# Kernel tuning notes

Hardware: AMD Instinct MI355X
Metric: run time of the kernel (lower is better)

## Reference

```python
import jax, jax.numpy as jnp
import numpy as np

N = 100000      # nodes
E = 3200000     # edges (avg degree 32)
G = 64          # graphs in batch
IN_C = 128      # in_channels
HID = 16        # hidden_channels
OUT_C = 8       # out_channels
EDGE_C = 16     # edge_channels


def setup_inputs() -> dict:
    key = jax.random.key(0)
    ks = jax.random.split(key, 10)
    x = jax.random.normal(ks[0], (N, IN_C), dtype=jnp.float32)
    edge_index = jax.random.randint(ks[1], (2, E), 0, N, dtype=jnp.int64)
    edge_attr = jax.random.normal(ks[2], (E, EDGE_C), dtype=jnp.float32)
    batch_index = jnp.sort(jax.random.randint(ks[3], (N,), 0, G, dtype=jnp.int64))
    def lin(k, fan_in, fan_out):
        bound = 1.0 / np.sqrt(fan_in)
        return jax.random.uniform(k, (fan_in, fan_out), jnp.float32, -bound, bound)
    return {
        "x": x,
        "edge_index": edge_index,
        "edge_attr": edge_attr,
        "batch_index": batch_index,
        "W1_node": lin(ks[4], IN_C, HID),
        "W1_edge": lin(ks[5], EDGE_C, HID),
        "W2_node": lin(ks[6], HID, HID),
        "W2_edge": lin(ks[7], EDGE_C, HID),
        "node_W": lin(ks[8], HID, OUT_C),
        "node_b": jax.random.uniform(ks[9], (OUT_C,), jnp.float32, -1.0 / np.sqrt(HID), 1.0 / np.sqrt(HID)),
    }


def _gcn_conv(h, edge_attr_pad, src, dst, norm, W_node, W_edge, n_nodes):
    # node/edge linear transforms (no bias, as in lin_node/lin_edge)
    node_emb = h @ W_node                       # [N, H]
    edge_emb = edge_attr_pad @ W_edge           # [E+N, H]
    # message: norm * (x_j + edge_attr), scatter-add at destination
    msg = norm[:, None] * (node_emb[src] + edge_emb)
    return jax.ops.segment_sum(msg, dst, num_segments=n_nodes)


def reference(x, edge_index, edge_attr, batch_index,
              W1_node, W1_edge, W2_node, W2_edge, node_W, node_b):
    n = x.shape[0]
    loop = jnp.arange(n, dtype=edge_index.dtype)
    src = jnp.concatenate([edge_index[0], loop])          # add_self_loops
    dst = jnp.concatenate([edge_index[1], loop])
    ea = jnp.concatenate(
        [edge_attr, jnp.zeros((n, edge_attr.shape[1]), edge_attr.dtype)], axis=0)
    # symmetric gcn_norm: deg from target index, norm = d^-1/2[src]*d^-1/2[dst]
    deg = jax.ops.segment_sum(jnp.ones_like(src, dtype=x.dtype), dst, num_segments=n)
    dinv = jnp.where(deg > 0, jax.lax.rsqrt(jnp.maximum(deg, 1.0)), 0.0)
    norm = dinv[src] * dinv[dst]

    h = jax.nn.relu(_gcn_conv(x, ea, src, dst, norm, W1_node, W1_edge, n))
    h = jax.nn.relu(_gcn_conv(h, ea, src, dst, norm, W2_node, W2_edge, n))

    # global mean pool over graphs
    ones = jnp.ones((n,), x.dtype)
    counts = jax.ops.segment_sum(ones, batch_index, num_segments=G)
    pooled = jax.ops.segment_sum(h, batch_index, num_segments=G)
    pooled = pooled / jnp.maximum(counts, 1.0)[:, None]

    return pooled @ node_W + node_b
```

## Files before the change

### kernel.cpp

```cpp
#include <hip/hip_runtime.h>
#include <hip/hip_bf16.h>

#define IN_C   128
#define HID    16
#define OUT_C  8
#define EDGE_C 16
#define NG     64
#define NRANGE 8

__global__ void deg_kernel(const int* __restrict__ dst, int* __restrict__ deg, int E) {
    int e = blockIdx.x * blockDim.x + threadIdx.x;
    if (e < E) atomicAdd(&deg[dst[e]], 1);
}

__global__ void scanA_kernel(const int* __restrict__ deg, int* __restrict__ row_start,
                             int* __restrict__ blocksum, int n) {
    __shared__ int s[256];
    int t = threadIdx.x;
    int i = blockIdx.x * 256 + t;
    int own = (i < n) ? deg[i] : 0;
    s[t] = own; __syncthreads();
    for (int off = 1; off < 256; off <<= 1) {
        int v = (t >= off) ? s[t - off] : 0;
        __syncthreads();
        s[t] += v;
        __syncthreads();
    }
    if (i < n) row_start[i] = s[t] - own;
    if (t == 255) blocksum[blockIdx.x] = s[255];
}

__global__ void scanB_kernel(int* __restrict__ blocksum, int nb) {
    __shared__ int s[512];
    int t = threadIdx.x;
    int own = (t < nb) ? blocksum[t] : 0;
    s[t] = own; __syncthreads();
    for (int off = 1; off < 512; off <<= 1) {
        int v = (t >= off) ? s[t - off] : 0;
        __syncthreads();
        s[t] += v;
        __syncthreads();
    }
    if (t < nb) blocksum[t] = s[t] - own;
}

__global__ void scanC_kernel(const int* __restrict__ deg, int* __restrict__ row_start,
                             const int* __restrict__ blocksum,
                             int* __restrict__ cursor, float* __restrict__ dinv, int n) {
    int i = blockIdx.x * 256 + threadIdx.x;
    if (i < n) {
        int rs = row_start[i] + blocksum[blockIdx.x];
        row_start[i] = rs;
        cursor[i] = rs;
        dinv[i] = rsqrtf((float)deg[i] + 1.0f);
    }
}

__global__ void fill_kernel(const int* __restrict__ src, const int* __restrict__ dst,
                            int* __restrict__ cursor, int2* __restrict__ adj,
                            int E, int range_size, int bpr) {
    int r = blockIdx.x & (NRANGE - 1);
    int q = blockIdx.x >> 3;
    int lo = r * range_size;
    int hi = lo + range_size;
    long long chunk = ((long long)E + bpr - 1) / bpr;
    int e0 = (int)((long long)q * chunk);
    long long e1l = (long long)e0 + chunk;
    int e1 = (e1l < E) ? (int)e1l : E;
    for (int e = e0 + threadIdx.x; e < e1; e += blockDim.x) {
        int d = dst[e];
        if (d >= lo && d < hi) {
            int pos = atomicAdd(&cursor[d], 1);
            adj[pos] = make_int2(e, src[e]);
        }
    }
}

__global__ void xform1_kernel(const float* __restrict__ x, const float* __restrict__ W,
                              const float* __restrict__ dinv, float* __restrict__ a1, int n) {
    int t = threadIdx.x;
    int v = blockIdx.x * 16 + (t >> 4);
    int c = t & 15;
    if (v >= n) return;
    const float4* xr = (const float4*)(x + (size_t)v * IN_C);
    float acc = 0.0f;
#pragma unroll
    for (int k4 = 0; k4 < IN_C / 4; ++k4) {
        float4 xv = xr[k4];
        int k = k4 * 4;
        acc += xv.x * W[(k + 0) * HID + c];
        acc += xv.y * W[(k + 1) * HID + c];
        acc += xv.z * W[(k + 2) * HID + c];
        acc += xv.w * W[(k + 3) * HID + c];
    }
    a1[(size_t)v * HID + c] = dinv[v] * acc;
}

__global__ void gather1_kernel(const int2* __restrict__ adj, const int* __restrict__ row_start,
                               const int* __restrict__ deg,
                               const float* __restrict__ edge_attr,
                               const float* __restrict__ W1e, const float* __restrict__ W2n,
                               const float* __restrict__ a1, const float* __restrict__ dinv,
                               float* __restrict__ a2, float* __restrict__ ES, int n) {
    int t = threadIdx.x;
    int lane = t & 63;
    int slot = lane >> 4;
    int c = lane & 15;
    float we[EDGE_C], wn[HID];
#pragma unroll
    for (int k = 0; k < EDGE_C; ++k) we[k] = W1e[k * HID + c];
#pragma unroll
    for (int k = 0; k < HID; ++k) wn[k] = W2n[k * HID + c];
    int v = blockIdx.x * 4 + (t >> 6);
    if (v >= n) return;
    int start = row_start[v];
    int dg = deg[v];
    float es = 0.0f, s1 = 0.0f;
    for (int i = slot; i < dg; i += 4) {
        int2 ad = adj[start + i];
        float ea = edge_attr[(size_t)ad.x * EDGE_C + c];
        float ds = dinv[ad.y];
        float av = a1[(size_t)ad.y * HID + c];
        es += ds * ea;
        s1 += av;
    }
    es += __shfl_xor(es, 16, 64); es += __shfl_xor(es, 32, 64);
    s1 += __shfl_xor(s1, 16, 64); s1 += __shfl_xor(s1, 32, 64);
    float dv = dinv[v];
    int lanebase = lane & ~15;
    float e1 = 0.0f;
#pragma unroll
    for (int k = 0; k < EDGE_C; ++k)
        e1 += __shfl(es, lanebase + k, 64) * we[k];
    float h = fmaxf(dv * (s1 + a1[(size_t)v * HID + c] + e1), 0.0f);
    float o = 0.0f;
#pragma unroll
    for (int k = 0; k < HID; ++k)
        o += __shfl(h, lanebase + k, 64) * wn[k];
    if (slot == 0) {
        a2[(size_t)v * HID + c] = dv * o;
        ES[(size_t)v * HID + c] = es;
    }
}

__global__ void gather2_kernel(const int2* __restrict__ adj, const int* __restrict__ row_start,
                               const int* __restrict__ deg,
                               const float* __restrict__ W2e,
                               const float* __restrict__ a2, const float* __restrict__ dinv,
                               const float* __restrict__ ES, float* __restrict__ h2, int n) {
    int t = threadIdx.x;
    int lane = t & 63;
    int slot = lane >> 4;
    int c = lane & 15;
    float we[EDGE_C];
#pragma unroll
    for (int k = 0; k < EDGE_C; ++k) we[k] = W2e[k * HID + c];
    int v = blockIdx.x * 4 + (t >> 6);
    if (v >= n) return;
    int start = row_start[v];
    int dg = deg[v];
    float s2 = 0.0f;
    for (int i = slot; i < dg; i += 4) {
        int2 ad = adj[start + i];
        s2 += a2[(size_t)ad.y * HID + c];
    }
    s2 += __shfl_xor(s2, 16, 64); s2 += __shfl_xor(s2, 32, 64);
    float dv = dinv[v];
    int lanebase = lane & ~15;
    float esv = ES[(size_t)v * HID + c];
    float e2 = 0.0f;
#pragma unroll
    for (int k = 0; k < EDGE_C; ++k)
        e2 += __shfl(esv, lanebase + k, 64) * we[k];
    float h = fmaxf(dv * (s2 + a2[(size_t)v * HID + c] + e2), 0.0f);
    if (slot == 0) h2[(size_t)v * HID + c] = h;
}

__global__ void pool_final_kernel(const float* __restrict__ h2,
                                  const int* __restrict__ batch,
                                  const float* __restrict__ W, const float* __restrict__ b,
                                  float* __restrict__ out, int n) {
    __shared__ float sdata[256];
    int g = blockIdx.x;
    int t = threadIdx.x;
    int c = t & 15;
    int lo = 0, hi = n;
    while (lo < hi) { int m = (lo + hi) >> 1; if (batch[m] < g) lo = m + 1; else hi = m; }
    int start = lo;
    hi = n;
    while (lo < hi) { int m = (lo + hi) >> 1; if (batch[m] < g + 1) lo = m + 1; else hi = m; }
    int end = lo;
    float acc = 0.0f;
    for (int v = start + (t >> 4); v < end; v += 16)
        acc += h2[(size_t)v * HID + c];
    sdata[t] = acc; __syncthreads();
    for (int s = 128; s >= 16; s >>= 1) {
        if (t < s) sdata[t] += sdata[t + s];
        __syncthreads();
    }
    if (t < OUT_C) {
        float inv = 1.0f / fmaxf((float)(end - start), 1.0f);
        float o = b[t];
#pragma unroll
        for (int cc = 0; cc < HID; ++cc)
            o += sdata[cc] * inv * W[cc * OUT_C + t];
        out[g * OUT_C + t] = o;
    }
}

extern "C" void kernel_launch(void* const* d_in, const int* in_sizes, int n_in,
                              void* d_out, int out_size, void* d_ws, size_t ws_size,
                              hipStream_t stream) {
    const float* x         = (const float*)d_in[0];
    const int*   edge_idx  = (const int*)d_in[1];
    const float* edge_attr = (const float*)d_in[2];
    const int*   batch     = (const int*)d_in[3];
    const float* W1_node   = (const float*)d_in[4];
    const float* W1_edge   = (const float*)d_in[5];
    const float* W2_node   = (const float*)d_in[6];
    const float* W2_edge   = (const float*)d_in[7];
    const float* node_W    = (const float*)d_in[8];
    const float* node_b    = (const float*)d_in[9];
    float* out = (float*)d_out;

    const int N = in_sizes[0] / IN_C;
    const int E = in_sizes[1] / 2;
    const int* src = edge_idx;
    const int* dst = edge_idx + E;

    char* p = (char*)d_ws;
    int2*  adj       = (int2*)p;   p += sizeof(int2) * (size_t)E;
    int*   deg       = (int*)p;    p += sizeof(int) * (size_t)N;
    int*   row_start = (int*)p;    p += sizeof(int) * (size_t)N;
    int*   cursor    = (int*)p;    p += sizeof(int) * (size_t)N;
    int*   blocksum  = (int*)p;    p += sizeof(int) * 512;
    float* dinv      = (float*)p;  p += sizeof(float) * (size_t)N;
    float* a1        = (float*)p;  p += sizeof(float) * (size_t)HID * N;
    float* a2        = (float*)p;  p += sizeof(float) * (size_t)HID * N;
    float* ES        = (float*)p;  p += sizeof(float) * (size_t)HID * N;
    float* h2        = a1;

    hipMemsetAsync(deg, 0, sizeof(int) * (size_t)N, stream);

    const int tb = 256;
    const int nbN = (N + 255) / 256;
    deg_kernel <<<(E + tb - 1) / tb, tb, 0, stream>>>(dst, deg, E);
    scanA_kernel<<<nbN, 256, 0, stream>>>(deg, row_start, blocksum, N);
    scanB_kernel<<<1, 512, 0, stream>>>(blocksum, nbN);
    scanC_kernel<<<nbN, 256, 0, stream>>>(deg, row_start, blocksum, cursor, dinv, N);

    const int range_size = (N + NRANGE - 1) / NRANGE;
    const int bpr = 128;
    fill_kernel<<<NRANGE * bpr, tb, 0, stream>>>(src, dst, cursor, adj, E, range_size, bpr);

    xform1_kernel<<<(N + 15) / 16, tb, 0, stream>>>(x, W1_node, dinv, a1, N);

    gather1_kernel<<<(N + 3) / 4, tb, 0, stream>>>(
        adj, row_start, deg, edge_attr, W1_edge, W2_node, a1, dinv, a2, ES, N);
    gather2_kernel<<<(N + 3) / 4, tb, 0, stream>>>(
        adj, row_start, deg, W2_edge, a2, dinv, ES, h2, N);

    pool_final_kernel<<<NG, 256, 0, stream>>>(h2, batch, node_W, node_b, out, N);
}
```

Measured before the change: 920.3 us.

## Pre-scale and permute edge attributes into CSR order during adjacency fill

When workspace allows, the fill kernel writes a per-slot copy of edge attributes scaled by dinv[src] in CSR order, plus a compact src index array. The gather kernels then read these contiguously and prefetch the next neighbor index. This aims to replace random edge_attr gathers and per-edge dinv lookups with streaming reads, at the cost of an extra large write of the permuted attributes during fill. A fallback keeps the original path when workspace is too small.

Result: slower. 1.110 ms (+20.6%).

```diff
diff --git a/kernel.cpp b/kernel.cpp
--- a/kernel.cpp
+++ b/kernel.cpp
@@ -56,9 +56,175 @@
     }
 }
 
-__global__ void fill_kernel(const int* __restrict__ src, const int* __restrict__ dst,
-                            int* __restrict__ cursor, int2* __restrict__ adj,
-                            int E, int range_size, int bpr) {
+__global__ void xform1_kernel(const float* __restrict__ x, const float* __restrict__ W,
+                              const float* __restrict__ dinv, float* __restrict__ a1, int n) {
+    int t = threadIdx.x;
+    int v = blockIdx.x * 16 + (t >> 4);
+    int c = t & 15;
+    if (v >= n) return;
+    const float4* xr = (const float4*)(x + (size_t)v * IN_C);
+    float acc = 0.0f;
+#pragma unroll
+    for (int k4 = 0; k4 < IN_C / 4; ++k4) {
+        float4 xv = xr[k4];
+        int k = k4 * 4;
+        acc += xv.x * W[(k + 0) * HID + c];
+        acc += xv.y * W[(k + 1) * HID + c];
+        acc += xv.z * W[(k + 2) * HID + c];
+        acc += xv.w * W[(k + 3) * HID + c];
+    }
+    a1[(size_t)v * HID + c] = dinv[v] * acc;
+}
+
+__global__ void pool_final_kernel(const float* __restrict__ h2,
+                                  const int* __restrict__ batch,
+                                  const float* __restrict__ W, const float* __restrict__ b,
+                                  float* __restrict__ out, int n) {
+    __shared__ float sdata[256];
+    int g = blockIdx.x;
+    int t = threadIdx.x;
+    int c = t & 15;
+    int lo = 0, hi = n;
+    while (lo < hi) { int m = (lo + hi) >> 1; if (batch[m] < g) lo = m + 1; else hi = m; }
+    int start = lo;
+    hi = n;
+    while (lo < hi) { int m = (lo + hi) >> 1; if (batch[m] < g + 1) lo = m + 1; else hi = m; }
+    int end = lo;
+    float acc = 0.0f;
+    for (int v = start + (t >> 4); v < end; v += 16)
+        acc += h2[(size_t)v * HID + c];
+    sdata[t] = acc; __syncthreads();
+    for (int s = 128; s >= 16; s >>= 1) {
+        if (t < s) sdata[t] += sdata[t + s];
+        __syncthreads();
+    }
+    if (t < OUT_C) {
+        float inv = 1.0f / fmaxf((float)(end - start), 1.0f);
+        float o = b[t];
+#pragma unroll
+        for (int cc = 0; cc < HID; ++cc)
+            o += sdata[cc] * inv * W[cc * OUT_C + t];
+        out[g * OUT_C + t] = o;
+    }
+}
+
+__global__ void fillW_kernel(const int* __restrict__ src, const int* __restrict__ dst,
+                             const float* __restrict__ edge_attr, const float* __restrict__ dinv,
+                             int* __restrict__ cursor, int* __restrict__ adjsrc,
+                             float* __restrict__ wea, int E, int range_size, int bpr) {
+    int r = blockIdx.x & (NRANGE - 1);
+    int q = blockIdx.x >> 3;
+    int lo = r * range_size;
+    int hi = lo + range_size;
+    long long chunk = ((long long)E + bpr - 1) / bpr;
+    int e0 = (int)((long long)q * chunk);
+    long long e1l = (long long)e0 + chunk;
+    int e1 = (e1l < E) ? (int)e1l : E;
+    for (int e = e0 + threadIdx.x; e < e1; e += blockDim.x) {
+        int d = dst[e];
+        if (d >= lo && d < hi) {
+            int s = src[e];
+            int pos = atomicAdd(&cursor[d], 1);
+            adjsrc[pos] = s;
+            float ds = dinv[s];
+            const float4* ea = (const float4*)(edge_attr + (size_t)e * EDGE_C);
+            float4* wr = (float4*)(wea + (size_t)pos * EDGE_C);
+            float4 v0 = ea[0], v1 = ea[1], v2 = ea[2], v3 = ea[3];
+            v0.x *= ds; v0.y *= ds; v0.z *= ds; v0.w *= ds;
+            v1.x *= ds; v1.y *= ds; v1.z *= ds; v1.w *= ds;
+            v2.x *= ds; v2.y *= ds; v2.z *= ds; v2.w *= ds;
+            v3.x *= ds; v3.y *= ds; v3.z *= ds; v3.w *= ds;
+            wr[0] = v0; wr[1] = v1; wr[2] = v2; wr[3] = v3;
+        }
+    }
+}
+
+__global__ void gather1W_kernel(const int* __restrict__ adjsrc, const int* __restrict__ row_start,
+                                const int* __restrict__ deg,
+                                const float* __restrict__ wea,
+                                const float* __restrict__ W1e, const float* __restrict__ W2n,
+                                const float* __restrict__ a1, const float* __restrict__ dinv,
+                                float* __restrict__ a2, float* __restrict__ ES, int n) {
+    int t = threadIdx.x;
+    int lane = t & 63;
+    int slot = lane >> 4;
+    int c = lane & 15;
+    float we[EDGE_C], wn[HID];
+#pragma unroll
+    for (int k = 0; k < EDGE_C; ++k) we[k] = W1e[k * HID + c];
+#pragma unroll
+    for (int k = 0; k < HID; ++k) wn[k] = W2n[k * HID + c];
+    int v = blockIdx.x * 4 + (t >> 6);
+    if (v >= n) return;
+    int start = row_start[v];
+    int dg = deg[v];
+    float es = 0.0f, s1 = 0.0f;
+    int i = slot;
+    int s_next = (i < dg) ? adjsrc[start + i] : 0;
+    for (; i < dg; i += 4) {
+        int s = s_next;
+        if (i + 4 < dg) s_next = adjsrc[start + i + 4];
+        es += wea[(size_t)(start + i) * HID + c];
+        s1 += a1[(size_t)s * HID + c];
+    }
+    es += __shfl_xor(es, 16, 64); es += __shfl_xor(es, 32, 64);
+    s1 += __shfl_xor(s1, 16, 64); s1 += __shfl_xor(s1, 32, 64);
+    float dv = dinv[v];
+    int lanebase = lane & ~15;
+    float e1 = 0.0f;
+#pragma unroll
+    for (int k = 0; k < EDGE_C; ++k)
+        e1 += __shfl(es, lanebase + k, 64) * we[k];
+    float h = fmaxf(dv * (s1 + a1[(size_t)v * HID + c] + e1), 0.0f);
+    float o = 0.0f;
+#pragma unroll
+    for (int k = 0; k < HID; ++k)
+        o += __shfl(h, lanebase + k, 64) * wn[k];
+    if (slot == 0) {
+        a2[(size_t)v * HID + c] = dv * o;
+        ES[(size_t)v * HID + c] = es;
+    }
+}
+
+__global__ void gather2W_kernel(const int* __restrict__ adjsrc, const int* __restrict__ row_start,
+                                const int* __restrict__ deg,
+                                const float* __restrict__ W2e,
+                                const float* __restrict__ a2, const float* __restrict__ dinv,
+                                const float* __restrict__ ES, float* __restrict__ h2, int n) {
+    int t = threadIdx.x;
+    int lane = t & 63;
+    int slot = lane >> 4;
+    int c = lane & 15;
+    float we[EDGE_C];
+#pragma unroll
+    for (int k = 0; k < EDGE_C; ++k) we[k] = W2e[k * HID + c];
+    int v = blockIdx.x * 4 + (t >> 6);
+    if (v >= n) return;
+    int start = row_start[v];
+    int dg = deg[v];
+    float s2 = 0.0f;
+    int i = slot;
+    int s_next = (i < dg) ? adjsrc[start + i] : 0;
+    for (; i < dg; i += 4) {
+        int s = s_next;
+        if (i + 4 < dg) s_next = adjsrc[start + i + 4];
+        s2 += a2[(size_t)s * HID + c];
+    }
+    s2 += __shfl_xor(s2, 16, 64); s2 += __shfl_xor(s2, 32, 64);
+    float dv = dinv[v];
+    int lanebase = lane & ~15;
+    float esv = ES[(size_t)v * HID + c];
+    float e2 = 0.0f;
+#pragma unroll
+    for (int k = 0; k < EDGE_C; ++k)
+        e2 += __shfl(esv, lanebase + k, 64) * we[k];
+    float h = fmaxf(dv * (s2 + a2[(size_t)v * HID + c] + e2), 0.0f);
+    if (slot == 0) h2[(size_t)v * HID + c] = h;
+}
+
+__global__ void fillF_kernel(const int* __restrict__ src, const int* __restrict__ dst,
+                             int* __restrict__ cursor, int2* __restrict__ adj,
+                             int E, int range_size, int bpr) {
     int r = blockIdx.x & (NRANGE - 1);
     int q = blockIdx.x >> 3;
     int lo = r * range_size;
@@ -76,32 +242,12 @@
     }
 }
 
-__global__ void xform1_kernel(const float* __restrict__ x, const float* __restrict__ W,
-                              const float* __restrict__ dinv, float* __restrict__ a1, int n) {
-    int t = threadIdx.x;
-    int v = blockIdx.x * 16 + (t >> 4);
-    int c = t & 15;
-    if (v >= n) return;
-    const float4* xr = (const float4*)(x + (size_t)v * IN_C);
-    float acc = 0.0f;
-#pragma unroll
-    for (int k4 = 0; k4 < IN_C / 4; ++k4) {
-        float4 xv = xr[k4];
-        int k = k4 * 4;
-        acc += xv.x * W[(k + 0) * HID + c];
-        acc += xv.y * W[(k + 1) * HID + c];
-        acc += xv.z * W[(k + 2) * HID + c];
-        acc += xv.w * W[(k + 3) * HID + c];
-    }
-    a1[(size_t)v * HID + c] = dinv[v] * acc;
-}
-
-__global__ void gather1_kernel(const int2* __restrict__ adj, const int* __restrict__ row_start,
-                               const int* __restrict__ deg,
-                               const float* __restrict__ edge_attr,
-                               const float* __restrict__ W1e, const float* __restrict__ W2n,
-                               const float* __restrict__ a1, const float* __restrict__ dinv,
-                               float* __restrict__ a2, float* __restrict__ ES, int n) {
+__global__ void gather1F_kernel(const int2* __restrict__ adj, const int* __restrict__ row_start,
+                                const int* __restrict__ deg,
+                                const float* __restrict__ edge_attr,
+                                const float* __restrict__ W1e, const float* __restrict__ W2n,
+                                const float* __restrict__ a1, const float* __restrict__ dinv,
+                                float* __restrict__ a2, float* __restrict__ ES, int n) {
     int t = threadIdx.x;
     int lane = t & 63;
     int slot = lane >> 4;
@@ -143,11 +289,11 @@
     }
 }
 
-__global__ void gather2_kernel(const int2* __restrict__ adj, const int* __restrict__ row_start,
-                               const int* __restrict__ deg,
-                               const float* __restrict__ W2e,
-                               const float* __restrict__ a2, const float* __restrict__ dinv,
-                               const float* __restrict__ ES, float* __restrict__ h2, int n) {
+__global__ void gather2F_kernel(const int2* __restrict__ adj, const int* __restrict__ row_start,
+                                const int* __restrict__ deg,
+                                const float* __restrict__ W2e,
+                                const float* __restrict__ a2, const float* __restrict__ dinv,
+                                const float* __restrict__ ES, float* __restrict__ h2, int n) {
     int t = threadIdx.x;
     int lane = t & 63;
     int slot = lane >> 4;
@@ -174,38 +320,6 @@
         e2 += __shfl(esv, lanebase + k, 64) * we[k];
     float h = fmaxf(dv * (s2 + a2[(size_t)v * HID + c] + e2), 0.0f);
     if (slot == 0) h2[(size_t)v * HID + c] = h;
-}
-
-__global__ void pool_final_kernel(const float* __restrict__ h2,
-                                  const int* __restrict__ batch,
-                                  const float* __restrict__ W, const float* __restrict__ b,
-                                  float* __restrict__ out, int n) {
-    __shared__ float sdata[256];
-    int g = blockIdx.x;
-    int t = threadIdx.x;
-    int c = t & 15;
-    int lo = 0, hi = n;
-    while (lo < hi) { int m = (lo + hi) >> 1; if (batch[m] < g) lo = m + 1; else hi = m; }
-    int start = lo;
-    hi = n;
-    while (lo < hi) { int m = (lo + hi) >> 1; if (batch[m] < g + 1) lo = m + 1; else hi = m; }
-    int end = lo;
-    float acc = 0.0f;
-    for (int v = start + (t >> 4); v < end; v += 16)
-        acc += h2[(size_t)v * HID + c];
-    sdata[t] = acc; __syncthreads();
-    for (int s = 128; s >= 16; s >>= 1) {
-        if (t < s) sdata[t] += sdata[t + s];
-        __syncthreads();
-    }
-    if (t < OUT_C) {
-        float inv = 1.0f / fmaxf((float)(end - start), 1.0f);
-        float o = b[t];
-#pragma unroll
-        for (int cc = 0; cc < HID; ++cc)
-            o += sdata[cc] * inv * W[cc * OUT_C + t];
-        out[g * OUT_C + t] = o;
-    }
 }
 
 extern "C" void kernel_launch(void* const* d_in, const int* in_sizes, int n_in,
@@ -228,37 +342,68 @@
     const int* src = edge_idx;
     const int* dst = edge_idx + E;
 
-    char* p = (char*)d_ws;
-    int2*  adj       = (int2*)p;   p += sizeof(int2) * (size_t)E;
-    int*   deg       = (int*)p;    p += sizeof(int) * (size_t)N;
-    int*   row_start = (int*)p;    p += sizeof(int) * (size_t)N;
-    int*   cursor    = (int*)p;    p += sizeof(int) * (size_t)N;
-    int*   blocksum  = (int*)p;    p += sizeof(int) * 512;
-    float* dinv      = (float*)p;  p += sizeof(float) * (size_t)N;
-    float* a1        = (float*)p;  p += sizeof(float) * (size_t)HID * N;
-    float* a2        = (float*)p;  p += sizeof(float) * (size_t)HID * N;
-    float* ES        = (float*)p;  p += sizeof(float) * (size_t)HID * N;
-    float* h2        = a1;
-
-    hipMemsetAsync(deg, 0, sizeof(int) * (size_t)N, stream);
-
     const int tb = 256;
     const int nbN = (N + 255) / 256;
-    deg_kernel <<<(E + tb - 1) / tb, tb, 0, stream>>>(dst, deg, E);
-    scanA_kernel<<<nbN, 256, 0, stream>>>(deg, row_start, blocksum, N);
-    scanB_kernel<<<1, 512, 0, stream>>>(blocksum, nbN);
-    scanC_kernel<<<nbN, 256, 0, stream>>>(deg, row_start, blocksum, cursor, dinv, N);
-
     const int range_size = (N + NRANGE - 1) / NRANGE;
     const int bpr = 128;
-    fill_kernel<<<NRANGE * bpr, tb, 0, stream>>>(src, dst, cursor, adj, E, range_size, bpr);
-
-    xform1_kernel<<<(N + 15) / 16, tb, 0, stream>>>(x, W1_node, dinv, a1, N);
-
-    gather1_kernel<<<(N + 3) / 4, tb, 0, stream>>>(
-        adj, row_start, deg, edge_attr, W1_edge, W2_node, a1, dinv, a2, ES, N);
-    gather2_kernel<<<(N + 3) / 4, tb, 0, stream>>>(
-        adj, row_start, deg, W2_edge, a2, dinv, ES, h2, N);
-
-    pool_final_kernel<<<NG, 256, 0, stream>>>(h2, batch, node_W, node_b, out, N);
-}
+
+    size_t needA = sizeof(float) * (size_t)EDGE_C * E
+                 + sizeof(int) * (size_t)E
+                 + sizeof(int) * (size_t)3 * N + 2048
+                 + sizeof(float) * (size_t)N
+                 + sizeof(float) * (size_t)3 * HID * N;
+
+    if (ws_size >= needA) {
+        char* p = (char*)d_ws;
+        float* wea      = (float*)p;  p += sizeof(float) * (size_t)EDGE_C * E;
+        int*   adjsrc   = (int*)p;    p += sizeof(int) * (size_t)E;
+        int*   deg      = (int*)p;    p += sizeof(int) * (size_t)N;
+        int*   row_start= (int*)p;    p += sizeof(int) * (size_t)N;
+        int*   cursor   = (int*)p;    p += sizeof(int) * (size_t)N;
+        int*   blocksum = (int*)p;    p += 2048;
+        float* dinv     = (float*)p;  p += sizeof(float) * (size_t)N;
+        float* a1       = (float*)p;  p += sizeof(float) * (size_t)HID * N;
+        float* a2       = (float*)p;  p += sizeof(float) * (size_t)HID * N;
+        float* ES       = (float*)p;  p += sizeof(float) * (size_t)HID * N;
+        float* h2 = a1;
+
+        hipMemsetAsync(deg, 0, sizeof(int) * (size_t)N, stream);
+        deg_kernel <<<(E + tb - 1) / tb, tb, 0, stream>>>(dst, deg, E);
+        scanA_kernel<<<nbN, 256, 0, stream>>>(deg, row_start, blocksum, N);
+        scanB_kernel<<<1, 512, 0, stream>>>(blocksum, nbN);
+        scanC_kernel<<<nbN, 256, 0, stream>>>(deg, row_start, blocksum, cursor, dinv, N);
+        fillW_kernel<<<NRANGE * bpr, tb, 0, stream>>>(src, dst, edge_attr, dinv,
+                                                      cursor, adjsrc, wea, E, range_size, bpr);
+        xform1_kernel<<<(N + 15) / 16, tb, 0, stream>>>(x, W1_node, dinv, a1, N);
+        gather1W_kernel<<<(N + 3) / 4, tb, 0, stream>>>(
+            adjsrc, row_start, deg, wea, W1_edge, W2_node, a1, dinv, a2, ES, N);
+        gather2W_kernel<<<(N + 3) / 4, tb, 0, stream>>>(
+            adjsrc, row_start, deg, W2_edge, a2, dinv, ES, h2, N);
+        pool_final_kernel<<<NG, 256, 0, stream>>>(h2, batch, node_W, node_b, out, N);
+    } else {
+        char* p = (char*)d_ws;
+        int2*  adj      = (int2*)p;   p += sizeof(int2) * (size_t)E;
+        int*   deg      = (int*)p;    p += sizeof(int) * (size_t)N;
+        int*   row_start= (int*)p;    p += sizeof(int) * (size_t)N;
+        int*   cursor   = (int*)p;    p += sizeof(int) * (size_t)N;
+        int*   blocksum = (int*)p;    p += 2048;
+        float* dinv     = (float*)p;  p += sizeof(float) * (size_t)N;
+        float* a1       = (float*)p;  p += sizeof(float) * (size_t)HID * N;
+        float* a2       = (float*)p;  p += sizeof(float) * (size_t)HID * N;
+        float* ES       = (float*)p;  p += sizeof(float) * (size_t)HID * N;
+        float* h2 = a1;
+
+        hipMemsetAsync(deg, 0, sizeof(int) * (size_t)N, stream);
+        deg_kernel <<<(E + tb - 1) / tb, tb, 0, stream>>>(dst, deg, E);
+        scanA_kernel<<<nbN, 256, 0, stream>>>(deg, row_start, blocksum, N);
+        scanB_kernel<<<1, 512, 0, stream>>>(blocksum, nbN);
+        scanC_kernel<<<nbN, 256, 0, stream>>>(deg, row_start, blocksum, cursor, dinv, N);
+        fillF_kernel<<<NRANGE * bpr, tb, 0, stream>>>(src, dst, cursor, adj, E, range_size, bpr);
+        xform1_kernel<<<(N + 15) / 16, tb, 0, stream>>>(x, W1_node, dinv, a1, N);
+        gather1F_kernel<<<(N + 3) / 4, tb, 0, stream>>>(
+            adj, row_start, deg, edge_attr, W1_edge, W2_node, a1, dinv, a2, ES, N);
+        gather2F_kernel<<<(N + 3) / 4, tb, 0, stream>>>(
+            adj, row_start, deg, W2_edge, a2, dinv, ES, h2, N);
+        pool_final_kernel<<<NG, 256, 0, stream>>>(h2, batch, node_W, node_b, out, N);
+    }
+}
```

## Range-partition degree atomics, split fill into two passes, prefetch adjacency in gathers

Applied to the files above, without the earlier changes.

The degree count now uses range-partitioned blocks, so each block only issues atomics for destinations in one of 16 node ranges, which keeps the atomic targets L2-resident. The CSR fill is split into two launches covering 8 ranges each, for the same locality reason. Both gather kernels unroll the neighbour loop by two and software-prefetch the next adjacency entries to raise memory-level parallelism. The cost is that dst is read many more times (16x for the degree pass, and 16x in total across the two fill passes) and there is one extra kernel launch.

Result: no change. 928.0 us (+0.8%).

```diff
diff --git a/kernel.cpp b/kernel.cpp
--- a/kernel.cpp
+++ b/kernel.cpp
@@ -6,11 +6,23 @@
 #define OUT_C  8
 #define EDGE_C 16
 #define NG     64
-#define NRANGE 8
-
-__global__ void deg_kernel(const int* __restrict__ dst, int* __restrict__ deg, int E) {
-    int e = blockIdx.x * blockDim.x + threadIdx.x;
-    if (e < E) atomicAdd(&deg[dst[e]], 1);
+#define NRANGE   16
+#define FILL_PR  8
+
+__global__ void deg_part_kernel(const int* __restrict__ dst, int* __restrict__ deg,
+                                int E, int range_size, int bpr) {
+    int r = blockIdx.x & (NRANGE - 1);
+    int q = blockIdx.x >> 4;
+    int lo = r * range_size;
+    int hi = lo + range_size;
+    long long chunk = ((long long)E + bpr - 1) / bpr;
+    int e0 = (int)((long long)q * chunk);
+    long long e1l = (long long)e0 + chunk;
+    int e1 = (e1l < E) ? (int)e1l : E;
+    for (int e = e0 + threadIdx.x; e < e1; e += blockDim.x) {
+        int d = dst[e];
+        if (d >= lo && d < hi) atomicAdd(&deg[d], 1);
+    }
 }
 
 __global__ void scanA_kernel(const int* __restrict__ deg, int* __restrict__ row_start,
@@ -58,8 +70,8 @@
 
 __global__ void fill_kernel(const int* __restrict__ src, const int* __restrict__ dst,
                             int* __restrict__ cursor, int2* __restrict__ adj,
-                            int E, int range_size, int bpr) {
-    int r = blockIdx.x & (NRANGE - 1);
+                            int E, int range_size, int bpr, int pass) {
+    int r = (blockIdx.x & (FILL_PR - 1)) + pass * FILL_PR;
     int q = blockIdx.x >> 3;
     int lo = r * range_size;
     int hi = lo + range_size;
@@ -116,13 +128,22 @@
     int start = row_start[v];
     int dg = deg[v];
     float es = 0.0f, s1 = 0.0f;
-    for (int i = slot; i < dg; i += 4) {
-        int2 ad = adj[start + i];
-        float ea = edge_attr[(size_t)ad.x * EDGE_C + c];
-        float ds = dinv[ad.y];
-        float av = a1[(size_t)ad.y * HID + c];
-        es += ds * ea;
-        s1 += av;
+    int i = slot;
+    int2 ad0 = (i     < dg) ? adj[start + i]     : make_int2(0, 0);
+    int2 ad1 = (i + 4 < dg) ? adj[start + i + 4] : make_int2(0, 0);
+    for (; i < dg; i += 8) {
+        int2 nad0 = (i +  8 < dg) ? adj[start + i +  8] : make_int2(0, 0);
+        int2 nad1 = (i + 12 < dg) ? adj[start + i + 12] : make_int2(0, 0);
+        float ea0 = edge_attr[(size_t)ad0.x * EDGE_C + c];
+        float a10 = a1[(size_t)ad0.y * HID + c];
+        float ds0 = dinv[ad0.y];
+        bool  ok1 = (i + 4 < dg);
+        float ea1 = ok1 ? edge_attr[(size_t)ad1.x * EDGE_C + c] : 0.0f;
+        float a11 = ok1 ? a1[(size_t)ad1.y * HID + c] : 0.0f;
+        float ds1 = ok1 ? dinv[ad1.y] : 0.0f;
+        es += ds0 * ea0 + ds1 * ea1;
+        s1 += a10 + a11;
+        ad0 = nad0; ad1 = nad1;
     }
     es += __shfl_xor(es, 16, 64); es += __shfl_xor(es, 32, 64);
     s1 += __shfl_xor(s1, 16, 64); s1 += __shfl_xor(s1, 32, 64);
@@ -160,9 +181,17 @@
     int start = row_start[v];
     int dg = deg[v];
     float s2 = 0.0f;
-    for (int i = slot; i < dg; i += 4) {
-        int2 ad = adj[start + i];
-        s2 += a2[(size_t)ad.y * HID + c];
+    int i = slot;
+    int2 ad0 = (i     < dg) ? adj[start + i]     : make_int2(0, 0);
+    int2 ad1 = (i + 4 < dg) ? adj[start + i + 4] : make_int2(0, 0);
+    for (; i < dg; i += 8) {
+        int2 nad0 = (i +  8 < dg) ? adj[start + i +  8] : make_int2(0, 0);
+        int2 nad1 = (i + 12 < dg) ? adj[start + i + 12] : make_int2(0, 0);
+        float v0 = a2[(size_t)ad0.y * HID + c];
+        bool  ok1 = (i + 4 < dg);
+        float v1 = ok1 ? a2[(size_t)ad1.y * HID + c] : 0.0f;
+        s2 += v0 + v1;
+        ad0 = nad0; ad1 = nad1;
     }
     s2 += __shfl_xor(s2, 16, 64); s2 += __shfl_xor(s2, 32, 64);
     float dv = dinv[v];
@@ -229,29 +258,33 @@
     const int* dst = edge_idx + E;
 
     char* p = (char*)d_ws;
-    int2*  adj       = (int2*)p;   p += sizeof(int2) * (size_t)E;
-    int*   deg       = (int*)p;    p += sizeof(int) * (size_t)N;
-    int*   row_start = (int*)p;    p += sizeof(int) * (size_t)N;
-    int*   cursor    = (int*)p;    p += sizeof(int) * (size_t)N;
-    int*   blocksum  = (int*)p;    p += sizeof(int) * 512;
-    float* dinv      = (float*)p;  p += sizeof(float) * (size_t)N;
-    float* a1        = (float*)p;  p += sizeof(float) * (size_t)HID * N;
-    float* a2        = (float*)p;  p += sizeof(float) * (size_t)HID * N;
-    float* ES        = (float*)p;  p += sizeof(float) * (size_t)HID * N;
-    float* h2        = a1;
+    int2*  adj      = (int2*)p;   p += sizeof(int2) * (size_t)E;
+    int*   deg      = (int*)p;    p += sizeof(int) * (size_t)N;
+    int*   row_start= (int*)p;    p += sizeof(int) * (size_t)N;
+    int*   cursor   = (int*)p;    p += sizeof(int) * (size_t)N;
+    int*   blocksum = (int*)p;    p += 2048;
+    float* dinv     = (float*)p;  p += sizeof(float) * (size_t)N;
+    float* a1       = (float*)p;  p += sizeof(float) * (size_t)HID * N;
+    float* a2       = (float*)p;  p += sizeof(float) * (size_t)HID * N;
+    float* ES       = (float*)p;  p += sizeof(float) * (size_t)HID * N;
+    float* h2 = a1;
 
     hipMemsetAsync(deg, 0, sizeof(int) * (size_t)N, stream);
 
     const int tb = 256;
     const int nbN = (N + 255) / 256;
-    deg_kernel <<<(E + tb - 1) / tb, tb, 0, stream>>>(dst, deg, E);
+    const int range_size = (N + NRANGE - 1) / NRANGE;
+
+    const int bprD = 64;
+    deg_part_kernel<<<NRANGE * bprD, tb, 0, stream>>>(dst, deg, E, range_size, bprD);
+
     scanA_kernel<<<nbN, 256, 0, stream>>>(deg, row_start, blocksum, N);
     scanB_kernel<<<1, 512, 0, stream>>>(blocksum, nbN);
     scanC_kernel<<<nbN, 256, 0, stream>>>(deg, row_start, blocksum, cursor, dinv, N);
 
-    const int range_size = (N + NRANGE - 1) / NRANGE;
-    const int bpr = 128;
-    fill_kernel<<<NRANGE * bpr, tb, 0, stream>>>(src, dst, cursor, adj, E, range_size, bpr);
+    const int bprF = 128;
+    fill_kernel<<<FILL_PR * bprF, tb, 0, stream>>>(src, dst, cursor, adj, E, range_size, bprF, 0);
+    fill_kernel<<<FILL_PR * bprF, tb, 0, stream>>>(src, dst, cursor, adj, E, range_size, bprF, 1);
 
     xform1_kernel<<<(N + 15) / 16, tb, 0, stream>>>(x, W1_node, dinv, a1, N);
 
```
